# Kernel tuning notes

Measured on AMD Instinct MI355X. Metric: run time of the kernel, lower is better.

## Reference

```python
import jax, jax.numpy as jnp
import numpy as np

B, C, H, W = 8, 64, 512, 512
KY = KX = 13


def setup_inputs() -> dict:
    key = jax.random.key(0)
    x = jax.random.normal(key, (B, C, H, W), dtype=jnp.float32)
    # BoxBlur buffer: get_box_kernel2d -> (1, ky, kx) filled with 1/(ky*kx)
    kernel = jnp.full((1, KY, KX), 1.0 / (KY * KX), dtype=jnp.float32)
    return {"input": x, "kernel": kernel}


def reference(input, kernel):
    # filter2d(input, kernel, border_type='reflect', padding='same', kind='corr')
    b, c, h, w = input.shape
    _, ky, kx = kernel.shape
    # _compute_padding: front = (k-1)//2, rear = (k-1) - front
    pt = (ky - 1) // 2
    pb = (ky - 1) - pt
    pl = (kx - 1) // 2
    pr = (kx - 1) - pl
    xp = jnp.pad(input, ((0, 0), (0, 0), (pt, pb), (pl, pr)), mode="reflect")
    # depthwise (grouped) correlation: rhs (C, 1, ky, kx), groups = C
    rhs = jnp.broadcast_to(kernel[:, None, :, :], (c, 1, ky, kx))
    out = jax.lax.conv_general_dilated(
        xp,
        rhs,
        window_strides=(1, 1),
        padding="VALID",
        dimension_numbers=("NCHW", "OIHW", "NCHW"),
        feature_group_count=c,
    )
    return out  # (B, C, H, W)
```

## Files before the change

### kernel.cpp

```cpp
#include <hip/hip_runtime.h>

#define IMG_H 512
#define IMG_W 512
#define TX 64
#define TY 64
#define HALO 12
#define IN_ROWS (TY + HALO)
#define IN_COLS (TX + HALO)
#define IN_STRIDE 77
#define HS_STRIDE 65

__global__ __launch_bounds__(256) void boxblur_kernel(
    const float* __restrict__ in, const float* __restrict__ kern,
    float* __restrict__ out) {
    __shared__ float in_s[IN_ROWS * IN_STRIDE];
    __shared__ float h_s[IN_ROWS * HS_STRIDE];

    const int tid = threadIdx.x;
    const int x0 = blockIdx.x * TX;
    const int y0 = blockIdx.y * TY;
    const size_t plane = (size_t)blockIdx.z * (IMG_H * IMG_W);
    const float* __restrict__ inp = in + plane;
    float* __restrict__ outp = out + plane;

    for (int li = tid; li < IN_ROWS * IN_COLS; li += 256) {
        int r = li / IN_COLS;
        int c = li - r * IN_COLS;
        int gy = y0 - 6 + r;
        gy = gy < 0 ? -gy : (gy >= IMG_H ? 2 * IMG_H - 2 - gy : gy);
        int gx = x0 - 6 + c;
        gx = gx < 0 ? -gx : (gx >= IMG_W ? 2 * IMG_W - 2 - gx : gx);
        in_s[r * IN_STRIDE + c] = inp[(size_t)gy * IMG_W + gx];
    }
    __syncthreads();

    for (int task = tid; task < IN_ROWS * 4; task += 256) {
        int r = task % IN_ROWS;
        int seg = task / IN_ROWS;
        int xs = seg * 16;
        const float* rowp = &in_s[r * IN_STRIDE];
        float* hrow = &h_s[r * HS_STRIDE];
        float s = 0.f;
        #pragma unroll
        for (int j = 0; j < 13; ++j) s += rowp[xs + j];
        hrow[xs] = s;
        #pragma unroll
        for (int x = 1; x < 16; ++x) {
            s += rowp[xs + x + 12] - rowp[xs + x - 1];
            hrow[xs + x] = s;
        }
    }
    __syncthreads();

    {
        const int col = tid & 63;
        const int seg = tid >> 6;
        const int ys = seg * 16;
        const float scale = kern[0];
        float s = 0.f;
        #pragma unroll
        for (int j = 0; j < 13; ++j) s += h_s[(ys + j) * HS_STRIDE + col];
        outp[(size_t)(y0 + ys) * IMG_W + x0 + col] = s * scale;
        #pragma unroll
        for (int dy = 1; dy < 16; ++dy) {
            int y = ys + dy;
            s += h_s[(y + 12) * HS_STRIDE + col] - h_s[(y - 1) * HS_STRIDE + col];
            outp[(size_t)(y0 + y) * IMG_W + x0 + col] = s * scale;
        }
    }
}

extern "C" void kernel_launch(void* const* d_in, const int* in_sizes, int n_in,
                              void* d_out, int out_size, void* d_ws, size_t ws_size,
                              hipStream_t stream) {
    const float* x = (const float*)d_in[0];
    const float* k = (const float*)d_in[1];
    float* out = (float*)d_out;
    dim3 grid(IMG_W / TX, IMG_H / TY, 8 * 64);
    dim3 block(256);
    boxblur_kernel<<<grid, block, 0, stream>>>(x, k, out);
}
```

Before: 957.6 us.

## Do vertical pass from global into registers, then horizontal, with float4 stores

Swaps the pass order. Each thread now loads a 28-row column strip straight from global memory into registers and runs the vertical running sum, so the staged input tile in shared memory is no longer needed. The horizontal pass then writes into a shared output tile, which is stored to global memory with float4 writes. This removes one full shared-memory staging round and vectorises the stores, at the cost of more registers per thread and column-strided global loads that are coalesced only across threads.

```diff
diff --git a/kernel.cpp b/kernel.cpp
--- a/kernel.cpp
+++ b/kernel.cpp
@@ -4,68 +4,79 @@
 #define IMG_W 512
 #define TX 64
 #define TY 64
-#define HALO 12
-#define IN_ROWS (TY + HALO)
-#define IN_COLS (TX + HALO)
-#define IN_STRIDE 77
-#define HS_STRIDE 65
+#define VCOLS 76
+#define VSTR 78
+#define OSTR 68
 
 __global__ __launch_bounds__(256) void boxblur_kernel(
     const float* __restrict__ in, const float* __restrict__ kern,
     float* __restrict__ out) {
-    __shared__ float in_s[IN_ROWS * IN_STRIDE];
-    __shared__ float h_s[IN_ROWS * HS_STRIDE];
+    __shared__ float v_s[TY * VSTR];
+    __shared__ float o_s[TY * OSTR];
 
     const int tid = threadIdx.x;
     const int x0 = blockIdx.x * TX;
     const int y0 = blockIdx.y * TY;
-    const size_t plane = (size_t)blockIdx.z * (IMG_H * IMG_W);
+    const size_t plane = (size_t)blockIdx.z * (size_t)(IMG_H * IMG_W);
     const float* __restrict__ inp = in + plane;
-    float* __restrict__ outp = out + plane;
 
-    for (int li = tid; li < IN_ROWS * IN_COLS; li += 256) {
-        int r = li / IN_COLS;
-        int c = li - r * IN_COLS;
-        int gy = y0 - 6 + r;
-        gy = gy < 0 ? -gy : (gy >= IMG_H ? 2 * IMG_H - 2 - gy : gy);
+    for (int task = tid; task < VCOLS * 4; task += 256) {
+        int c = task % VCOLS;
+        int s = task / VCOLS;
         int gx = x0 - 6 + c;
-        gx = gx < 0 ? -gx : (gx >= IMG_W ? 2 * IMG_W - 2 - gx : gx);
-        in_s[r * IN_STRIDE + c] = inp[(size_t)gy * IMG_W + gx];
-    }
-    __syncthreads();
-
-    for (int task = tid; task < IN_ROWS * 4; task += 256) {
-        int r = task % IN_ROWS;
-        int seg = task / IN_ROWS;
-        int xs = seg * 16;
-        const float* rowp = &in_s[r * IN_STRIDE];
-        float* hrow = &h_s[r * HS_STRIDE];
-        float s = 0.f;
+        gx = gx < 0 ? -gx : (gx > IMG_W - 1 ? 2 * (IMG_W - 1) - gx : gx);
+        int yb = y0 + s * 16;
+        float a[28];
         #pragma unroll
-        for (int j = 0; j < 13; ++j) s += rowp[xs + j];
-        hrow[xs] = s;
+        for (int k = 0; k < 28; ++k) {
+            int gy = yb - 6 + k;
+            gy = gy < 0 ? -gy : (gy > IMG_H - 1 ? 2 * (IMG_H - 1) - gy : gy);
+            a[k] = inp[(size_t)gy * IMG_W + gx];
+        }
+        float sum = 0.f;
         #pragma unroll
-        for (int x = 1; x < 16; ++x) {
-            s += rowp[xs + x + 12] - rowp[xs + x - 1];
-            hrow[xs + x] = s;
+        for (int k = 0; k < 13; ++k) sum += a[k];
+        v_s[(s * 16) * VSTR + c] = sum;
+        #pragma unroll
+        for (int t = 1; t < 16; ++t) {
+            sum += a[t + 12] - a[t - 1];
+            v_s[(s * 16 + t) * VSTR + c] = sum;
         }
     }
     __syncthreads();
 
     {
-        const int col = tid & 63;
-        const int seg = tid >> 6;
-        const int ys = seg * 16;
+        const int y = tid & 63;
+        const int s = tid >> 6;
+        const int xb = s * 16;
         const float scale = kern[0];
-        float s = 0.f;
+        const float* vrow = &v_s[y * VSTR + xb];
+        float* orow = &o_s[y * OSTR + xb];
+        float sum = 0.f;
         #pragma unroll
-        for (int j = 0; j < 13; ++j) s += h_s[(ys + j) * HS_STRIDE + col];
-        outp[(size_t)(y0 + ys) * IMG_W + x0 + col] = s * scale;
+        for (int j = 0; j < 13; ++j) sum += vrow[j];
+        orow[0] = sum * scale;
         #pragma unroll
-        for (int dy = 1; dy < 16; ++dy) {
-            int y = ys + dy;
-            s += h_s[(y + 12) * HS_STRIDE + col] - h_s[(y - 1) * HS_STRIDE + col];
-            outp[(size_t)(y0 + y) * IMG_W + x0 + col] = s * scale;
+        for (int t = 1; t < 16; ++t) {
+            sum += vrow[t + 12] - vrow[t - 1];
+            orow[t] = sum * scale;
+        }
+    }
+    __syncthreads();
+
+    {
+        float* __restrict__ outp = out + plane;
+        const int g = tid & 15;
+        const int seg = tid >> 4;
+        #pragma unroll
+        for (int i = 0; i < 4; ++i) {
+            int r = seg * 4 + i;
+            float4 v;
+            v.x = o_s[r * OSTR + 4 * g + 0];
+            v.y = o_s[r * OSTR + 4 * g + 1];
+            v.z = o_s[r * OSTR + 4 * g + 2];
+            v.w = o_s[r * OSTR + 4 * g + 3];
+            *(float4*)(outp + (size_t)(y0 + r) * IMG_W + x0 + 4 * g) = v;
         }
     }
 }
```

Result: faster. 868.6 us (-9.3%).
